# Kernel tuning notes

Measured on AMD Instinct MI355X. Metric: run time of the kernel, lower is better.

The kernel has to match this reference:

```python
import jax, jax.numpy as jnp
import numpy as np

N_NODES = 100000
N_EDGES = 1600000
F_IN = 128
F_OUT = 64


def setup_inputs() -> dict:
    key = jax.random.key(0)
    k1, k2, k3, k4 = jax.random.split(key, 4)
    node_features = jax.random.normal(k1, (N_NODES, F_IN), dtype=jnp.float32)
    edge_index = jax.random.randint(k2, (2, N_EDGES), 0, N_NODES, dtype=jnp.int32)
    edge_weight = jax.random.uniform(k3, (N_EDGES,), dtype=jnp.float32)
    W = jax.random.normal(k4, (F_IN, F_OUT), dtype=jnp.float32) * (1.0 / np.sqrt(F_IN))
    b = jnp.zeros((F_OUT,), dtype=jnp.float32)
    return {"node_features": node_features, "edge_index": edge_index,
            "edge_weight": edge_weight, "W": W, "b": b}


def reference(node_features, edge_index, edge_weight, W, b):
    # GCNConv: x' = D^{-1/2} (A + I) D^{-1/2} (X W) + b, edge-weighted.
    n = node_features.shape[0]
    row, col = edge_index[0], edge_index[1]  # source, target
    # add self-loops with weight 1
    loop = jnp.arange(n, dtype=edge_index.dtype)
    row_f = jnp.concatenate([row, loop])
    col_f = jnp.concatenate([col, loop])
    w_f = jnp.concatenate([edge_weight, jnp.ones((n,), edge_weight.dtype)])
    # symmetric normalization
    deg = jax.ops.segment_sum(w_f, col_f, num_segments=n)  # [N]
    dis = jnp.where(deg > 0, jax.lax.rsqrt(deg), 0.0)      # deg^{-1/2}
    norm = dis[row_f] * w_f * dis[col_f]                   # [E+N]
    # transform then scatter-aggregate messages at targets
    xw = node_features @ W                                  # [N, F_OUT]
    msgs = norm[:, None] * xw[row_f]                        # [E+N, F_OUT]
    out = jax.ops.segment_sum(msgs, col_f, num_segments=n)  # [N, F_OUT]
    out = out + b
    # ReLU; dropout(p=0.001) is identity in inference mode
    return jax.nn.relu(out)
```

## Files before the change

kernel.cpp:

```cpp
#include <hip/hip_runtime.h>

#define F_IN 128
#define F_OUT 64
#define LSTR 136
#define EB 4096
#define BSH 8
#define BNODES 256
#define BCAP 4608
#define QCAP 1536

typedef __bf16 bf16x8 __attribute__((ext_vector_type(8)));
typedef float f32x4 __attribute__((ext_vector_type(4)));

__device__ inline ushort f2bf(float f) {
    unsigned u = __float_as_uint(f);
    return (ushort)((u + 0x7fff + ((u >> 16) & 1)) >> 16);
}
__device__ inline float bf2f(ushort u) { return __uint_as_float((unsigned)u << 16); }

__global__ __launch_bounds__(512) void k_scatter_gemm(
        const float* __restrict__ X, const float* __restrict__ W,
        const int* __restrict__ ei, const float* __restrict__ ew,
        unsigned* __restrict__ bcnt, unsigned* __restrict__ sortedA,
        unsigned char* __restrict__ cl, ushort* __restrict__ xwb,
        int n, int e, int nblk, int nbuck) {
    __shared__ union SM {
        struct {
            unsigned srt[EB];
            unsigned meta[EB];
            unsigned s[512];
            unsigned cnt[512];
            unsigned ptr[512];
            unsigned delta[512];
        } sc;
        ushort Wt[64 * LSTR];
    } sm;
    const int t = threadIdx.x;

    if ((int)blockIdx.x >= nblk) {
        ushort* Wt = sm.Wt;
        const int row0 = ((int)blockIdx.x - nblk) * 128;
        const float4* W4 = (const float4*)W;
        #pragma unroll
        for (int i = 0; i < 4; ++i) {
            int idx = t + i * 512;
            float4 v = W4[idx];
            int flat = idx * 4;
            int k = flat >> 6, c = flat & 63;
            Wt[(c + 0) * LSTR + k] = f2bf(v.x);
            Wt[(c + 1) * LSTR + k] = f2bf(v.y);
            Wt[(c + 2) * LSTR + k] = f2bf(v.z);
            Wt[(c + 3) * LSTR + k] = f2bf(v.w);
        }
        const int lane = t & 63, wv_ = t >> 6;
        const int m16 = lane & 15, quad = lane >> 4;
        int arow = row0 + wv_ * 16 + m16;
        if (arow >= n) arow = n - 1;
        const float* xr = X + (long)arow * F_IN;
        __syncthreads();

        f32x4 acc[4] = {{0,0,0,0},{0,0,0,0},{0,0,0,0},{0,0,0,0}};
        #pragma unroll
        for (int kk = 0; kk < 4; ++kk) {
            float4 xa = *(const float4*)(xr + kk * 32 + quad * 8);
            float4 xb = *(const float4*)(xr + kk * 32 + quad * 8 + 4);
            union { ushort us[8]; bf16x8 v; } ua;
            ua.us[0] = f2bf(xa.x); ua.us[1] = f2bf(xa.y);
            ua.us[2] = f2bf(xa.z); ua.us[3] = f2bf(xa.w);
            ua.us[4] = f2bf(xb.x); ua.us[5] = f2bf(xb.y);
            ua.us[6] = f2bf(xb.z); ua.us[7] = f2bf(xb.w);
            #pragma unroll
            for (int nt = 0; nt < 4; ++nt) {
                bf16x8 bb = *(const bf16x8*)&Wt[(nt * 16 + m16) * LSTR + kk * 32 + quad * 8];
                acc[nt] = __builtin_amdgcn_mfma_f32_16x16x32_bf16(ua.v, bb, acc[nt], 0, 0, 0);
            }
        }
        #pragma unroll
        for (int nt = 0; nt < 4; ++nt) {
            #pragma unroll
            for (int reg = 0; reg < 4; ++reg) {
                int gr = row0 + wv_ * 16 + quad * 4 + reg;
                if (gr < n) xwb[(long)gr * F_OUT + nt * 16 + m16] = f2bf(acc[nt][reg]);
            }
        }
        return;
    }

    const int blk = (int)blockIdx.x;
    sm.sc.cnt[t] = 0;
    __syncthreads();

    const int base = blk * EB;
    unsigned cc[EB / 512], rr[EB / 512], ww[EB / 512];
    #pragma unroll
    for (int jj = 0; jj < EB / 512; ++jj) {
        int i = base + jj * 512 + t;
        unsigned c = 0xffffffffu, r = 0, w15 = 0;
        if (i < e) {
            c = (unsigned)ei[e + i];
            r = (unsigned)ei[i];
            unsigned u = __float_as_uint(ew[i]);
            w15 = ((u + 0x7fff + ((u >> 16) & 1)) >> 16) & 0x7fffu;
            atomicAdd(&sm.sc.cnt[c >> BSH], 1u);
        }
        cc[jj] = c; rr[jj] = r; ww[jj] = w15;
    }
    __syncthreads();

    unsigned cv = sm.sc.cnt[t];
    sm.sc.s[t] = cv;
    __syncthreads();
    for (int off = 1; off < 512; off <<= 1) {
        unsigned u = (t >= off) ? sm.sc.s[t - off] : 0;
        __syncthreads();
        sm.sc.s[t] += u;
        __syncthreads();
    }
    const unsigned excl = sm.sc.s[t] - cv;
    sm.sc.ptr[t] = excl;
    unsigned rbase = (t < nbuck && cv > 0) ? atomicAdd(&bcnt[t], cv) : 0;
    sm.sc.delta[t] = (unsigned)t * BCAP + rbase - excl;
    __syncthreads();

    #pragma unroll
    for (int jj = 0; jj < EB / 512; ++jj) {
        if (cc[jj] != 0xffffffffu) {
            unsigned d = atomicAdd(&sm.sc.ptr[cc[jj] >> BSH], 1u);
            sm.sc.srt[d] = (rr[jj] << 15) | ww[jj];
            sm.sc.meta[d] = cc[jj];
        }
    }
    __syncthreads();

    const int cnum = (e - base < EB) ? (e - base) : EB;
    #pragma unroll
    for (int jj = 0; jj < EB / 512; ++jj) {
        int i = jj * 512 + t;
        if (i < cnum) {
            unsigned c = sm.sc.meta[i];
            unsigned bb = c >> BSH;
            unsigned dest = sm.sc.delta[bb] + (unsigned)i;
            if (dest < (bb + 1) * BCAP) {
                sortedA[dest] = sm.sc.srt[i];
                cl[dest] = (unsigned char)(c & (BNODES - 1));
            }
        }
    }
}

__global__ __launch_bounds__(256, 8) void k_deg(
        const unsigned* __restrict__ sortedA, const unsigned char* __restrict__ cl,
        const unsigned* __restrict__ bcnt, float* __restrict__ dis, int n) {
    __shared__ float dl[64];
    const int b = (int)blockIdx.x >> 2, qtr = (int)blockIdx.x & 3;
    const int t = threadIdx.x;
    const unsigned S = (unsigned)b * BCAP;
    unsigned bc = bcnt[b];
    const int seg = (int)(bc < BCAP ? bc : BCAP);
    if (t < 64) dl[t] = 0.f;
    __syncthreads();
    for (int j = t; j < seg; j += 256) {
        unsigned c0 = cl[S + j];
        if ((int)(c0 >> 6) == qtr) {
            unsigned r = sortedA[S + j];
            atomicAdd(&dl[c0 & 63], __uint_as_float((r & 0x7fffu) << 16));
        }
    }
    __syncthreads();
    int c = b * BNODES + qtr * 64 + t;
    if (t < 64 && c < n) dis[c] = rsqrtf(dl[t] + 1.0f);
}

__global__ __launch_bounds__(256, 8) void k_gather(
        const unsigned* __restrict__ sortedA, const unsigned char* __restrict__ cl,
        const unsigned* __restrict__ bcnt, const float* __restrict__ dis,
        const ushort* __restrict__ xwb, const float* __restrict__ bias,
        float* __restrict__ out, int n) {
    __shared__ unsigned srt[QCAP];
    __shared__ unsigned cnt[64];
    __shared__ unsigned offs[64];
    __shared__ unsigned ptr[64];
    const int b = (int)blockIdx.x >> 2, qtr = (int)blockIdx.x & 3;
    const int t = threadIdx.x;
    const unsigned S = (unsigned)b * BCAP;
    unsigned bc = bcnt[b];
    const int seg = (int)(bc < BCAP ? bc : BCAP);
    if (t < 64) cnt[t] = 0;
    __syncthreads();

    for (int j = t; j < seg; j += 256) {
        unsigned c0 = cl[S + j];
        if ((int)(c0 >> 6) == qtr) atomicAdd(&cnt[c0 & 63], 1u);
    }
    __syncthreads();
    if (t < 64) offs[t] = cnt[t];
    __syncthreads();
    for (int off = 1; off < 64; off <<= 1) {
        unsigned u = (t < 64 && t >= off) ? offs[t - off] : 0;
        __syncthreads();
        if (t < 64) offs[t] += u;
        __syncthreads();
    }
    if (t < 64) ptr[t] = offs[t] - cnt[t];
    __syncthreads();
    for (int j = t; j < seg; j += 256) {
        unsigned c0 = cl[S + j];
        if ((int)(c0 >> 6) == qtr) {
            unsigned d = atomicAdd(&ptr[c0 & 63], 1u);
            if (d < QCAP) srt[d] = sortedA[S + j];
        }
    }
    __syncthreads();

    const int wv = t >> 6, lane = t & 63, q = lane >> 4, fl = lane & 15;
    #pragma unroll 1
    for (int i = 0; i < 16; ++i) {
        int nl = wv * 16 + i;
        int node = b * BNODES + qtr * 64 + nl;
        if (node >= n) continue;
        float dc = dis[node];
        int end = (int)offs[nl];
        int beg = end - (int)cnt[nl];
        if (end > QCAP) end = QCAP;
        float a0 = 0.f, a1 = 0.f, a2 = 0.f, a3 = 0.f;
        if (q == 0) {
            ushort4 xv = *(const ushort4*)(xwb + (long)node * 64 + fl * 4);
            a0 = dc * bf2f(xv.x); a1 = dc * bf2f(xv.y);
            a2 = dc * bf2f(xv.z); a3 = dc * bf2f(xv.w);
        }
        for (int j = beg + q; j < end; j += 16) {
            bool m1 = j + 4 < end, m2 = j + 8 < end, m3 = j + 12 < end;
            int j1 = m1 ? j + 4 : j, j2 = m2 ? j + 8 : j, j3 = m3 ? j + 12 : j;
            unsigned v0 = srt[j],  v1 = srt[j1];
            unsigned v2 = srt[j2], v3 = srt[j3];
            int r0 = (int)(v0 >> 15), r1 = (int)(v1 >> 15);
            int r2 = (int)(v2 >> 15), r3 = (int)(v3 >> 15);
            float d0 = dis[r0], d1 = dis[r1], d2 = dis[r2], d3 = dis[r3];
            ushort4 x0 = *(const ushort4*)(xwb + (long)r0 * 64 + fl * 4);
            ushort4 x1 = *(const ushort4*)(xwb + (long)r1 * 64 + fl * 4);
            ushort4 x2 = *(const ushort4*)(xwb + (long)r2 * 64 + fl * 4);
            ushort4 x3 = *(const ushort4*)(xwb + (long)r3 * 64 + fl * 4);
            float w0 = __uint_as_float((v0 & 0x7fffu) << 16) * d0;
            float w1 = m1 ? __uint_as_float((v1 & 0x7fffu) << 16) * d1 : 0.f;
            float w2 = m2 ? __uint_as_float((v2 & 0x7fffu) << 16) * d2 : 0.f;
            float w3 = m3 ? __uint_as_float((v3 & 0x7fffu) << 16) * d3 : 0.f;
            a0 += w0 * bf2f(x0.x) + w1 * bf2f(x1.x) + w2 * bf2f(x2.x) + w3 * bf2f(x3.x);
            a1 += w0 * bf2f(x0.y) + w1 * bf2f(x1.y) + w2 * bf2f(x2.y) + w3 * bf2f(x3.y);
            a2 += w0 * bf2f(x0.z) + w1 * bf2f(x1.z) + w2 * bf2f(x2.z) + w3 * bf2f(x3.z);
            a3 += w0 * bf2f(x0.w) + w1 * bf2f(x1.w) + w2 * bf2f(x2.w) + w3 * bf2f(x3.w);
        }
        a0 += __shfl_xor(a0, 16); a0 += __shfl_xor(a0, 32);
        a1 += __shfl_xor(a1, 16); a1 += __shfl_xor(a1, 32);
        a2 += __shfl_xor(a2, 16); a2 += __shfl_xor(a2, 32);
        a3 += __shfl_xor(a3, 16); a3 += __shfl_xor(a3, 32);
        if (q == 0) {
            float4 bb = ((const float4*)bias)[fl];
            float f0 = dc * a0 + bb.x, f1 = dc * a1 + bb.y;
            float f2 = dc * a2 + bb.z, f3 = dc * a3 + bb.w;
            ((float4*)out)[(long)node * 16 + fl] =
                make_float4(f0 > 0.f ? f0 : 0.f, f1 > 0.f ? f1 : 0.f,
                            f2 > 0.f ? f2 : 0.f, f3 > 0.f ? f3 : 0.f);
        }
    }
}

extern "C" void kernel_launch(void* const* d_in, const int* in_sizes, int n_in,
                              void* d_out, int out_size, void* d_ws, size_t ws_size,
                              hipStream_t stream) {
    const float* X  = (const float*)d_in[0];
    const int*   ei = (const int*)d_in[1];
    const float* ew = (const float*)d_in[2];
    const float* W  = (const float*)d_in[3];
    const float* b  = (const float*)d_in[4];
    float* out = (float*)d_out;

    const int n = in_sizes[0] / F_IN;
    const int e = in_sizes[2];

    const int NBLK  = (e + EB - 1) / EB;
    const int NBUCK = (n + BNODES - 1) / BNODES;
    const int nb_gemm = (n + 127) / 128;

    long p = 0;
    auto alloc = [&](long bytes) { long off = p; p += (bytes + 255) & ~255L; return off; };
    char* ws = (char*)d_ws;
    long o_bcnt   = alloc((long)NBUCK * 4);
    long o_sorted = alloc((long)NBUCK * BCAP * 4);
    long o_cl     = alloc((long)NBUCK * BCAP);
    long o_dis    = alloc((long)n * 4);
    long o_xwb    = alloc((long)n * F_OUT * 2);
    unsigned*      bcnt    = (unsigned*)(ws + o_bcnt);
    unsigned*      sortedA = (unsigned*)(ws + o_sorted);
    unsigned char* cl      = (unsigned char*)(ws + o_cl);
    float*         dis     = (float*)(ws + o_dis);
    ushort*        xwb     = (ushort*)(ws + o_xwb);

    hipMemsetAsync(ws + o_bcnt, 0, (size_t)NBUCK * 4, stream);
    k_scatter_gemm<<<NBLK + nb_gemm, 512, 0, stream>>>(X, W, ei, ew, bcnt,
                                                       sortedA, cl, xwb,
                                                       n, e, NBLK, NBUCK);
    k_deg<<<NBUCK * 4, 256, 0, stream>>>(sortedA, cl, bcnt, dis, n);
    k_gather<<<NBUCK * 4, 256, 0, stream>>>(sortedA, cl, bcnt, dis, xwb,
                                            b, out, n);
}
```

Measured before the change: 192.6 us.

## Replace per-node CSR sort in gather with LDS atomic accumulation

The gather kernel no longer counts, prefix-scans and re-sorts edges per target node in shared memory. Instead it initialises a 64x64 float accumulator in LDS with the self-loop term, has groups of 16 threads process edges directly from the bucket and atomically add weighted messages into the accumulator, then applies normalisation, bias and ReLU. This removes several barriers and the counting/scan passes, but every qualifying edge now costs four LDS float atomics. Each block also scans the whole bucket segment, keeping only edges for its own quarter, so about three quarters of the edges each block reads are skipped.

```diff
diff --git a/kernel.cpp b/kernel.cpp
--- a/kernel.cpp
+++ b/kernel.cpp
@@ -7,7 +7,6 @@
 #define BSH 8
 #define BNODES 256
 #define BCAP 4608
-#define QCAP 1536
 
 typedef __bf16 bf16x8 __attribute__((ext_vector_type(8)));
 typedef float f32x4 __attribute__((ext_vector_type(4)));
@@ -176,88 +175,95 @@
         const unsigned* __restrict__ bcnt, const float* __restrict__ dis,
         const ushort* __restrict__ xwb, const float* __restrict__ bias,
         float* __restrict__ out, int n) {
-    __shared__ unsigned srt[QCAP];
-    __shared__ unsigned cnt[64];
-    __shared__ unsigned offs[64];
-    __shared__ unsigned ptr[64];
+    __shared__ float acc[64 * 64];
     const int b = (int)blockIdx.x >> 2, qtr = (int)blockIdx.x & 3;
     const int t = threadIdx.x;
     const unsigned S = (unsigned)b * BCAP;
+    const int nbase = b * BNODES + qtr * 64;
     unsigned bc = bcnt[b];
     const int seg = (int)(bc < BCAP ? bc : BCAP);
-    if (t < 64) cnt[t] = 0;
-    __syncthreads();
-
-    for (int j = t; j < seg; j += 256) {
-        unsigned c0 = cl[S + j];
-        if ((int)(c0 >> 6) == qtr) atomicAdd(&cnt[c0 & 63], 1u);
-    }
-    __syncthreads();
-    if (t < 64) offs[t] = cnt[t];
-    __syncthreads();
-    for (int off = 1; off < 64; off <<= 1) {
-        unsigned u = (t < 64 && t >= off) ? offs[t - off] : 0;
-        __syncthreads();
-        if (t < 64) offs[t] += u;
-        __syncthreads();
-    }
-    if (t < 64) ptr[t] = offs[t] - cnt[t];
-    __syncthreads();
-    for (int j = t; j < seg; j += 256) {
-        unsigned c0 = cl[S + j];
-        if ((int)(c0 >> 6) == qtr) {
-            unsigned d = atomicAdd(&ptr[c0 & 63], 1u);
-            if (d < QCAP) srt[d] = sortedA[S + j];
-        }
-    }
-    __syncthreads();
-
-    const int wv = t >> 6, lane = t & 63, q = lane >> 4, fl = lane & 15;
-    #pragma unroll 1
-    for (int i = 0; i < 16; ++i) {
-        int nl = wv * 16 + i;
-        int node = b * BNODES + qtr * 64 + nl;
-        if (node >= n) continue;
-        float dc = dis[node];
-        int end = (int)offs[nl];
-        int beg = end - (int)cnt[nl];
-        if (end > QCAP) end = QCAP;
-        float a0 = 0.f, a1 = 0.f, a2 = 0.f, a3 = 0.f;
-        if (q == 0) {
-            ushort4 xv = *(const ushort4*)(xwb + (long)node * 64 + fl * 4);
-            a0 = dc * bf2f(xv.x); a1 = dc * bf2f(xv.y);
-            a2 = dc * bf2f(xv.z); a3 = dc * bf2f(xv.w);
-        }
-        for (int j = beg + q; j < end; j += 16) {
-            bool m1 = j + 4 < end, m2 = j + 8 < end, m3 = j + 12 < end;
-            int j1 = m1 ? j + 4 : j, j2 = m2 ? j + 8 : j, j3 = m3 ? j + 12 : j;
-            unsigned v0 = srt[j],  v1 = srt[j1];
-            unsigned v2 = srt[j2], v3 = srt[j3];
-            int r0 = (int)(v0 >> 15), r1 = (int)(v1 >> 15);
-            int r2 = (int)(v2 >> 15), r3 = (int)(v3 >> 15);
-            float d0 = dis[r0], d1 = dis[r1], d2 = dis[r2], d3 = dis[r3];
-            ushort4 x0 = *(const ushort4*)(xwb + (long)r0 * 64 + fl * 4);
-            ushort4 x1 = *(const ushort4*)(xwb + (long)r1 * 64 + fl * 4);
-            ushort4 x2 = *(const ushort4*)(xwb + (long)r2 * 64 + fl * 4);
-            ushort4 x3 = *(const ushort4*)(xwb + (long)r3 * 64 + fl * 4);
-            float w0 = __uint_as_float((v0 & 0x7fffu) << 16) * d0;
-            float w1 = m1 ? __uint_as_float((v1 & 0x7fffu) << 16) * d1 : 0.f;
-            float w2 = m2 ? __uint_as_float((v2 & 0x7fffu) << 16) * d2 : 0.f;
-            float w3 = m3 ? __uint_as_float((v3 & 0x7fffu) << 16) * d3 : 0.f;
-            a0 += w0 * bf2f(x0.x) + w1 * bf2f(x1.x) + w2 * bf2f(x2.x) + w3 * bf2f(x3.x);
-            a1 += w0 * bf2f(x0.y) + w1 * bf2f(x1.y) + w2 * bf2f(x2.y) + w3 * bf2f(x3.y);
-            a2 += w0 * bf2f(x0.z) + w1 * bf2f(x1.z) + w2 * bf2f(x2.z) + w3 * bf2f(x3.z);
-            a3 += w0 * bf2f(x0.w) + w1 * bf2f(x1.w) + w2 * bf2f(x2.w) + w3 * bf2f(x3.w);
-        }
-        a0 += __shfl_xor(a0, 16); a0 += __shfl_xor(a0, 32);
-        a1 += __shfl_xor(a1, 16); a1 += __shfl_xor(a1, 32);
-        a2 += __shfl_xor(a2, 16); a2 += __shfl_xor(a2, 32);
-        a3 += __shfl_xor(a3, 16); a3 += __shfl_xor(a3, 32);
-        if (q == 0) {
-            float4 bb = ((const float4*)bias)[fl];
-            float f0 = dc * a0 + bb.x, f1 = dc * a1 + bb.y;
-            float f2 = dc * a2 + bb.z, f3 = dc * a3 + bb.w;
-            ((float4*)out)[(long)node * 16 + fl] =
+
+    for (int i = t; i < 64 * 16; i += 256) {
+        int nl = i >> 4, f4 = i & 15;
+        int node = nbase + nl;
+        float v0 = 0.f, v1 = 0.f, v2 = 0.f, v3 = 0.f;
+        if (node < n) {
+            float dc = dis[node];
+            ushort4 xv = *(const ushort4*)(xwb + (long)node * 64 + f4 * 4);
+            v0 = dc * bf2f(xv.x); v1 = dc * bf2f(xv.y);
+            v2 = dc * bf2f(xv.z); v3 = dc * bf2f(xv.w);
+        }
+        int a = nl * 64 + f4 * 4;
+        acc[a + 0] = v0; acc[a + 1] = v1; acc[a + 2] = v2; acc[a + 3] = v3;
+    }
+    __syncthreads();
+
+    const int qw = t >> 4, fl = t & 15;
+    for (int j0 = qw; j0 < seg; j0 += 64) {
+        int j1 = (j0 + 16 < seg) ? j0 + 16 : j0;
+        int j2 = (j0 + 32 < seg) ? j0 + 32 : j0;
+        int j3 = (j0 + 48 < seg) ? j0 + 48 : j0;
+        unsigned c0 = cl[S + j0], c1 = cl[S + j1];
+        unsigned c2 = cl[S + j2], c3 = cl[S + j3];
+        unsigned v0 = sortedA[S + j0], v1 = sortedA[S + j1];
+        unsigned v2 = sortedA[S + j2], v3 = sortedA[S + j3];
+        bool o0 = ((int)(c0 >> 6) == qtr);
+        bool o1 = (j0 + 16 < seg) && ((int)(c1 >> 6) == qtr);
+        bool o2 = (j0 + 32 < seg) && ((int)(c2 >> 6) == qtr);
+        bool o3 = (j0 + 48 < seg) && ((int)(c3 >> 6) == qtr);
+        if (o0) {
+            int r = (int)(v0 >> 15);
+            float w = __uint_as_float((v0 & 0x7fffu) << 16) * dis[r];
+            ushort4 x = *(const ushort4*)(xwb + (long)r * 64 + fl * 4);
+            int a = (int)(c0 & 63) * 64 + fl * 4;
+            atomicAdd(&acc[a + 0], w * bf2f(x.x));
+            atomicAdd(&acc[a + 1], w * bf2f(x.y));
+            atomicAdd(&acc[a + 2], w * bf2f(x.z));
+            atomicAdd(&acc[a + 3], w * bf2f(x.w));
+        }
+        if (o1) {
+            int r = (int)(v1 >> 15);
+            float w = __uint_as_float((v1 & 0x7fffu) << 16) * dis[r];
+            ushort4 x = *(const ushort4*)(xwb + (long)r * 64 + fl * 4);
+            int a = (int)(c1 & 63) * 64 + fl * 4;
+            atomicAdd(&acc[a + 0], w * bf2f(x.x));
+            atomicAdd(&acc[a + 1], w * bf2f(x.y));
+            atomicAdd(&acc[a + 2], w * bf2f(x.z));
+            atomicAdd(&acc[a + 3], w * bf2f(x.w));
+        }
+        if (o2) {
+            int r = (int)(v2 >> 15);
+            float w = __uint_as_float((v2 & 0x7fffu) << 16) * dis[r];
+            ushort4 x = *(const ushort4*)(xwb + (long)r * 64 + fl * 4);
+            int a = (int)(c2 & 63) * 64 + fl * 4;
+            atomicAdd(&acc[a + 0], w * bf2f(x.x));
+            atomicAdd(&acc[a + 1], w * bf2f(x.y));
+            atomicAdd(&acc[a + 2], w * bf2f(x.z));
+            atomicAdd(&acc[a + 3], w * bf2f(x.w));
+        }
+        if (o3) {
+            int r = (int)(v3 >> 15);
+            float w = __uint_as_float((v3 & 0x7fffu) << 16) * dis[r];
+            ushort4 x = *(const ushort4*)(xwb + (long)r * 64 + fl * 4);
+            int a = (int)(c3 & 63) * 64 + fl * 4;
+            atomicAdd(&acc[a + 0], w * bf2f(x.x));
+            atomicAdd(&acc[a + 1], w * bf2f(x.y));
+            atomicAdd(&acc[a + 2], w * bf2f(x.z));
+            atomicAdd(&acc[a + 3], w * bf2f(x.w));
+        }
+    }
+    __syncthreads();
+
+    for (int i = t; i < 64 * 16; i += 256) {
+        int nl = i >> 4, f4 = i & 15;
+        int node = nbase + nl;
+        if (node < n) {
+            float dc = dis[node];
+            float4 bb = ((const float4*)bias)[f4];
+            int a = nl * 64 + f4 * 4;
+            float f0 = dc * acc[a + 0] + bb.x, f1 = dc * acc[a + 1] + bb.y;
+            float f2 = dc * acc[a + 2] + bb.z, f3 = dc * acc[a + 3] + bb.w;
+            ((float4*)out)[(long)node * 16 + f4] =
                 make_float4(f0 > 0.f ? f0 : 0.f, f1 > 0.f ? f1 : 0.f,
                             f2 > 0.f ? f2 : 0.f, f3 > 0.f ? f3 : 0.f);
         }
```

Result: slower. 743.7 us (+286.1%).
